# Performance work log

Hardware: AMD Instinct MI355X
Metric: run time of the kernel (lower is better)

The kernel has to match this reference:

```python
import jax, jax.numpy as jnp
import numpy as np

B, D, K, H = 8192, 1024, 8, 2048


def setup_inputs() -> dict:
    key = jax.random.key(0)
    ks = jax.random.split(key, 4)
    x = jax.random.normal(ks[0], (B, D), dtype=jnp.float32)
    centroids = jax.random.normal(ks[1], (K, D), dtype=jnp.float32)
    W1 = jax.random.normal(ks[2], (K, D, H), dtype=jnp.float32) / np.sqrt(D).astype(np.float32)
    b1 = jnp.zeros((K, H), dtype=jnp.float32)
    W2 = jax.random.normal(ks[3], (K, H), dtype=jnp.float32) / np.sqrt(H).astype(np.float32)
    b2 = jnp.zeros((K,), dtype=jnp.float32)
    return {"x": x, "centroids": centroids, "W1": W1, "b1": b1, "W2": W2, "b2": b2}


def reference(x, centroids, W1, b1, W2, b2):
    # --- k-means hard routing: nearest centroid per sample (euclidean max_sim) ---
    # d2[b,k] = ||x_b||^2 - 2 x_b . c_k + ||c_k||^2  (avoid [B,K,D] blowup)
    d2 = (jnp.sum(x * x, axis=-1, keepdims=True)
          - 2.0 * (x @ centroids.T)
          + jnp.sum(centroids * centroids, axis=-1)[None, :])  # [B, K]
    cluster = jnp.argmin(d2, axis=-1)  # [B] int, hard assignment

    # --- per-expert log-likelihood heads (Einet stand-in), computed densely ---
    h = jnp.tanh(jnp.einsum("bd,kdh->kbh", x, W1) + b1[:, None, :])  # [K, B, H]
    lls = jnp.einsum("kbh,kh->kb", h, W2) + b2[:, None]              # [K, B]

    # --- combine: each sample takes the LL from its routed expert, original order ---
    lls_sorted = jnp.take_along_axis(lls.T, cluster[:, None], axis=1)[:, 0]  # [B]
    return lls_sorted
```

## Files before the change

### kernel.cpp

```cpp
#include <hip/hip_runtime.h>
#include <hip/hip_bf16.h>
#include <stdint.h>

#define B_N 8192
#define D_N 1024
#define K_N 8
#define H_N 2048

#define BM 160
#define BN 128
#define BK 64
#define NBLK 512
#define ABYTES 20480
#define BUFSZ 36864
#define RO_OFF 73728
#define PLL_OFF 74368
#define GEMM_LDS 75648

typedef unsigned int u32;
typedef unsigned short u16;
typedef __attribute__((ext_vector_type(8))) short short8;
typedef __attribute__((ext_vector_type(4))) float float4v;

struct __align__(8) us4 { u16 x, y, z, w; };

__device__ __forceinline__ u16 f2bf(float f) {
    union { float f; u32 u; } v; v.f = f;
    u32 u = v.u;
    u32 r = (u + 0x7fffu + ((u >> 16) & 1u)) >> 16;
    return (u16)r;
}

__device__ __forceinline__ float fast_tanh(float x) {
    float t = __expf(2.0f * x);
    return 1.0f - 2.0f * __builtin_amdgcn_rcpf(t + 1.0f);
}

__device__ __forceinline__ void async_copy16(void* lds, const void* g) {
    __builtin_amdgcn_global_load_lds(
        (const __attribute__((address_space(1))) void*)g,
        (__attribute__((address_space(3))) void*)lds, 16, 0, 0);
}

__global__ void route_kernel(const float* __restrict__ x,
                             const float* __restrict__ cent,
                             u16* __restrict__ xbf,
                             int* __restrict__ cluster,
                             u32* __restrict__ counts) {
    int tid = threadIdx.x;
    if (blockIdx.x == 0 && tid < K_N) counts[tid * 32] = 0;
    int wave = tid >> 6, lane = tid & 63;
    int b = blockIdx.x * 4 + wave;
    const float* xr = x + (size_t)b * D_N;

    float4 xv[4];
#pragma unroll
    for (int i = 0; i < 4; ++i)
        xv[i] = *(const float4*)(xr + i * 256 + lane * 4);

#pragma unroll
    for (int i = 0; i < 4; ++i) {
        us4 o;
        o.x = f2bf(xv[i].x); o.y = f2bf(xv[i].y);
        o.z = f2bf(xv[i].z); o.w = f2bf(xv[i].w);
        *(us4*)(xbf + (size_t)b * D_N + i * 256 + lane * 4) = o;
    }

    double acc[K_N];
#pragma unroll
    for (int k = 0; k < K_N; ++k) {
        const float* cr = cent + k * D_N;
        double s = 0.0;
#pragma unroll
        for (int i = 0; i < 4; ++i) {
            float4 cv = *(const float4*)(cr + i * 256 + lane * 4);
            double d0 = (double)xv[i].x - (double)cv.x; s += d0 * d0;
            double d1 = (double)xv[i].y - (double)cv.y; s += d1 * d1;
            double d2 = (double)xv[i].z - (double)cv.z; s += d2 * d2;
            double d3 = (double)xv[i].w - (double)cv.w; s += d3 * d3;
        }
        acc[k] = s;
    }
#pragma unroll
    for (int k = 0; k < K_N; ++k) {
        double v = acc[k];
        for (int off = 32; off; off >>= 1) v += __shfl_down(v, off);
        acc[k] = v;
    }
    if (lane == 0) {
        int best = 0; double bv = acc[0];
#pragma unroll
        for (int k = 1; k < K_N; ++k)
            if (acc[k] < bv) { bv = acc[k]; best = k; }
        cluster[b] = best;
    }
}

__global__ void scatter_kernel(const int* __restrict__ cluster,
                               u32* __restrict__ counts,
                               u32* __restrict__ idxl) {
    __shared__ u32 wcnt[4][K_N];
    __shared__ u32 gb[K_N];
    int tid = threadIdx.x;
    int b = blockIdx.x * 256 + tid;
    int lane = tid & 63, wid = tid >> 6;
    int cl = cluster[b];
    unsigned long long lower = (1ull << lane) - 1ull;
    u32 rank = 0;
#pragma unroll
    for (int k = 0; k < K_N; ++k) {
        unsigned long long mk = __ballot(cl == k);
        if (k == cl) rank = (u32)__popcll(mk & lower);
        if (lane == 0) wcnt[wid][k] = (u32)__popcll(mk);
    }
    __syncthreads();
    if (tid < K_N) {
        u32 tot = wcnt[0][tid] + wcnt[1][tid] + wcnt[2][tid] + wcnt[3][tid];
        gb[tid] = atomicAdd(&counts[tid * 32], tot);
    }
    __syncthreads();
    u32 woff = 0;
    if (wid > 0) woff += wcnt[0][cl];
    if (wid > 1) woff += wcnt[1][cl];
    if (wid > 2) woff += wcnt[2][cl];
    idxl[(size_t)cl * B_N + gb[cl] + woff + rank] = (u32)b;
}

__global__ void w1t_kernel(const float* __restrict__ w1, u16* __restrict__ w1t) {
    __shared__ float ts[64][65];
    int tid = threadIdx.x;
    int h0 = blockIdx.x * 64, d0 = blockIdx.y * 64, k = blockIdx.z;
    const float* src = w1 + ((size_t)k * D_N + d0) * H_N + h0;
#pragma unroll
    for (int i = 0; i < 4; ++i) {
        int q = i * 256 + tid;
        int r = q >> 4, c4 = (q & 15) * 4;
        float4 v = *(const float4*)(src + (size_t)r * H_N + c4);
        ts[c4 + 0][r] = v.x; ts[c4 + 1][r] = v.y;
        ts[c4 + 2][r] = v.z; ts[c4 + 3][r] = v.w;
    }
    __syncthreads();
    u16* dst = w1t + ((size_t)k * H_N + h0) * D_N + d0;
#pragma unroll
    for (int i = 0; i < 4; ++i) {
        int q = i * 256 + tid;
        int hr = q >> 4, d4 = (q & 15) * 4;
        us4 o;
        o.x = f2bf(ts[hr][d4 + 0]); o.y = f2bf(ts[hr][d4 + 1]);
        o.z = f2bf(ts[hr][d4 + 2]); o.w = f2bf(ts[hr][d4 + 3]);
        *(us4*)(dst + (size_t)hr * D_N + d4) = o;
    }
}

__global__ __launch_bounds__(256, 2) void gemm_kernel(
                            const u16* __restrict__ xbf,
                            const u16* __restrict__ w1t,
                            const float* __restrict__ b1,
                            const float* __restrict__ w2,
                            const u32* __restrict__ idxl,
                            const u32* __restrict__ counts,
                            float* __restrict__ llp) {
    extern __shared__ char lds[];
    int tid = threadIdx.x;
    int lane = tid & 63, w = tid >> 6;
    int wm = w >> 1, wn = w & 1;
    int wmbase = wm * 80;
    int l15 = lane & 15, l4 = lane >> 4;

    u32* ro = (u32*)(lds + RO_OFF);
    float* pll = (float*)(lds + PLL_OFF);

    int ntiles = 0;
#pragma unroll
    for (int kk = 0; kk < K_N; ++kk)
        ntiles += ((int)counts[kk * 32] + BM - 1) / BM;
    int total = ntiles * 16;

    int swz = l15 & 7;
    u32 aB0 = (u32)((wmbase + l15) * 128 + (((0 + l4) ^ swz) << 4));
    u32 aB1 = (u32)((wmbase + l15) * 128 + (((4 + l4) ^ swz) << 4));
    u32 bB0 = (u32)(ABYTES + (wn * 64 + l15) * 128 + (((0 + l4) ^ swz) << 4));
    u32 bB1 = (u32)(ABYTES + (wn * 64 + l15) * 128 + (((4 + l4) ^ swz) << 4));

    const char* xb = (const char*)xbf;
    const char* wb = (const char*)w1t;

#define BAR() do { asm volatile("" ::: "memory"); __builtin_amdgcn_s_barrier(); \
                   asm volatile("" ::: "memory"); } while (0)

    for (int item = blockIdx.x; item < total; item += NBLK) {
        int nc = ((item & 7) << 1) | ((item >> 3) & 1);
        int tile = item >> 4;
        int k = 0, mt = 0, nt = 0;
#pragma unroll
        for (int kk = 0; kk < K_N; ++kk) {
            int c = (int)counts[kk * 32];
            int t = (c + BM - 1) / BM;
            if (tile >= nt && tile < nt + t) { k = kk; mt = tile - nt; }
            nt += t;
        }
        int cnt = (int)counts[k * 32];
        int rows = cnt - mt * BM; if (rows > BM) rows = BM;
        int h0 = nc * BN;

        if (tid < BM) {
            int m = mt * BM + tid;
            int mm = m < cnt ? m : cnt - 1;
            ro[tid] = idxl[(size_t)k * B_N + mm] * (u32)(D_N * 2);
        }
        __syncthreads();

        u32 srcA[5], srcB[4];
#pragma unroll
        for (int i = 0; i < 5; ++i) {
            int c = i * 256 + tid; int r = c >> 3, j = c & 7;
            srcA[i] = ro[r] + ((u32)(j ^ (r & 7)) << 4);
        }
#pragma unroll
        for (int i = 0; i < 4; ++i) {
            int c = i * 256 + tid; int r = c >> 3, j = c & 7;
            srcB[i] = ((u32)(k * H_N + h0 + r) << 11) + ((u32)(j ^ (r & 7)) << 4);
        }

        float4v acc[5][4];
#pragma unroll
        for (int mf = 0; mf < 5; ++mf)
#pragma unroll
            for (int nf = 0; nf < 4; ++nf)
                acc[mf][nf] = (float4v){0.f, 0.f, 0.f, 0.f};

#pragma unroll
        for (int i = 0; i < 5; ++i)
            async_copy16(lds + i * 4096 + tid * 16, xb + srcA[i]);
#pragma unroll
        for (int i = 0; i < 4; ++i)
            async_copy16(lds + ABYTES + i * 4096 + tid * 16, wb + srcB[i]);

        for (int t = 0; t < 16; ++t) {
            const char* Acur = lds + (t & 1) * BUFSZ;
            char* Bnx = lds + ((t + 1) & 1) * BUFSZ;
            if (t < 15) {
                u32 d = (u32)((t + 1) << 7);
#pragma unroll
                for (int i = 0; i < 5; ++i)
                    async_copy16(Bnx + i * 4096 + tid * 16, xb + srcA[i] + d);
#pragma unroll
                for (int i = 0; i < 4; ++i)
                    async_copy16(Bnx + ABYTES + i * 4096 + tid * 16, wb + srcB[i] + d);
                asm volatile("s_waitcnt vmcnt(9)" ::: "memory");
            } else {
                asm volatile("s_waitcnt vmcnt(0)" ::: "memory");
            }
            BAR();
#pragma unroll
            for (int kk = 0; kk < 2; ++kk) {
                short8 bC[4], a[5];
                u32 aB = kk ? aB1 : aB0, bB = kk ? bB1 : bB0;
#pragma unroll
                for (int nf = 0; nf < 4; ++nf)
                    bC[nf] = *(const short8*)(Acur + bB + nf * 2048);
#pragma unroll
                for (int mf = 0; mf < 5; ++mf)
                    a[mf] = *(const short8*)(Acur + aB + mf * 2048);
                __builtin_amdgcn_s_setprio(1);
#pragma unroll
                for (int mf = 0; mf < 5; ++mf) {
                    if (wmbase + mf * 16 < rows) {
#pragma unroll
                        for (int nf = 0; nf < 4; ++nf)
                            acc[mf][nf] = __builtin_amdgcn_mfma_f32_16x16x32_bf16(
                                a[mf], bC[nf], acc[mf][nf], 0, 0, 0);
                    }
                }
                __builtin_amdgcn_s_setprio(0);
            }
            BAR();
        }

        float w2v[4], b1v[4];
#pragma unroll
        for (int nf = 0; nf < 4; ++nf) {
            int h = h0 + wn * 64 + nf * 16 + l15;
            w2v[nf] = w2[k * H_N + h];
            b1v[nf] = b1[k * H_N + h];
        }
#pragma unroll
        for (int mf = 0; mf < 5; ++mf) {
            float rs[4] = {0.f, 0.f, 0.f, 0.f};
#pragma unroll
            for (int nf = 0; nf < 4; ++nf) {
#pragma unroll
                for (int r = 0; r < 4; ++r)
                    rs[r] += fast_tanh(acc[mf][nf][r] + b1v[nf]) * w2v[nf];
            }
#pragma unroll
            for (int r = 0; r < 4; ++r) {
                float v = rs[r];
                v += __shfl_xor(v, 8);
                v += __shfl_xor(v, 4);
                v += __shfl_xor(v, 2);
                v += __shfl_xor(v, 1);
                if (l15 == 0) pll[wn * 160 + wmbase + mf * 16 + l4 * 4 + r] = v;
            }
        }
        __syncthreads();
        if (tid < BM) {
            int m = mt * BM + tid;
            if (m < cnt) {
                u32 b = idxl[(size_t)k * B_N + m];
                llp[(size_t)nc * B_N + b] = pll[tid] + pll[160 + tid];
            }
        }
        __syncthreads();
    }
#undef BAR
}

__global__ void combine_kernel(const float* __restrict__ llp,
                               const int* __restrict__ cluster,
                               const float* __restrict__ b2,
                               float* __restrict__ out) {
    int b = blockIdx.x * 256 + threadIdx.x;
    float s = b2[cluster[b]];
#pragma unroll
    for (int nc = 0; nc < 16; ++nc) s += llp[(size_t)nc * B_N + b];
    out[b] = s;
}

extern "C" void kernel_launch(void* const* d_in, const int* in_sizes, int n_in,
                              void* d_out, int out_size, void* d_ws, size_t ws_size,
                              hipStream_t stream) {
    const float* x    = (const float*)d_in[0];
    const float* cent = (const float*)d_in[1];
    const float* W1   = (const float*)d_in[2];
    const float* b1   = (const float*)d_in[3];
    const float* W2   = (const float*)d_in[4];
    const float* b2   = (const float*)d_in[5];
    float* out = (float*)d_out;

    char* ws = (char*)d_ws;
    u16* xbf     = (u16*)(ws + 0);
    u16* w1t     = (u16*)(ws + 16777216);
    u32* counts  = (u32*)(ws + 50331648);
    int* cluster = (int*)(ws + 50332672);
    u32* idxl    = (u32*)(ws + 50365440);
    float* llp   = (float*)(ws + 50627584);

    (void)hipFuncSetAttribute((const void*)gemm_kernel,
                              hipFuncAttributeMaxDynamicSharedMemorySize, GEMM_LDS);

    hipLaunchKernelGGL(route_kernel, dim3(B_N / 4), dim3(256), 0, stream,
                       x, cent, xbf, cluster, counts);
    hipLaunchKernelGGL(scatter_kernel, dim3(32), dim3(256), 0, stream,
                       cluster, counts, idxl);
    hipLaunchKernelGGL(w1t_kernel, dim3(H_N / 64, D_N / 64, K_N), dim3(256), 0, stream,
                       W1, w1t);
    hipLaunchKernelGGL(gemm_kernel, dim3(NBLK), dim3(256), GEMM_LDS, stream,
                       xbf, w1t, b1, W2, idxl, counts, llp);
    hipLaunchKernelGGL(combine_kernel, dim3(B_N / 256), dim3(256), 0, stream,
                       llp, cluster, b2, out);
}
```

Before: 95.87 us.

## Enlarge GEMM tiles to 288x256 with 8 waves and 4-stage half-K pipeline

The GEMM now uses 512-thread blocks with a 288x256 output tile and 32-wide K steps held in a four-deep LDS ring, prefetching two steps ahead. Loads for the next A and B half-stages are interleaved between two MFMA phases inside each step. Larger tiles mean fewer items and less duplicated global traffic for x and W1, and combine now sums 8 partials instead of 16. The trade-offs are higher register pressure from 9x4 accumulators, more LDS per block with fewer blocks resident, and more barriers per K step.

```diff
diff --git a/kernel.cpp b/kernel.cpp
--- a/kernel.cpp
+++ b/kernel.cpp
@@ -7,15 +7,14 @@
 #define K_N 8
 #define H_N 2048
 
-#define BM 160
-#define BN 128
-#define BK 64
-#define NBLK 512
-#define ABYTES 20480
-#define BUFSZ 36864
-#define RO_OFF 73728
-#define PLL_OFF 74368
-#define GEMM_LDS 75648
+#define BM 288
+#define BN 256
+#define NBLK 256
+#define ABYTES_HS 18432
+#define HSB 34816
+#define RO_OFF 139264
+#define PLL_OFF 140416
+#define GEMM_LDS 145024
 
 typedef unsigned int u32;
 typedef unsigned short u16;
@@ -152,7 +151,7 @@
     }
 }
 
-__global__ __launch_bounds__(256, 2) void gemm_kernel(
+__global__ __launch_bounds__(512, 2) void gemm_kernel(
                             const u16* __restrict__ xbf,
                             const u16* __restrict__ w1t,
                             const float* __restrict__ b1,
@@ -163,8 +162,8 @@
     extern __shared__ char lds[];
     int tid = threadIdx.x;
     int lane = tid & 63, w = tid >> 6;
-    int wm = w >> 1, wn = w & 1;
-    int wmbase = wm * 80;
+    int wm = w >> 2, wn = w & 3;
+    int wmbase = wm * 144;
     int l15 = lane & 15, l4 = lane >> 4;
 
     u32* ro = (u32*)(lds + RO_OFF);
@@ -174,23 +173,22 @@
 #pragma unroll
     for (int kk = 0; kk < K_N; ++kk)
         ntiles += ((int)counts[kk * 32] + BM - 1) / BM;
-    int total = ntiles * 16;
-
-    int swz = l15 & 7;
-    u32 aB0 = (u32)((wmbase + l15) * 128 + (((0 + l4) ^ swz) << 4));
-    u32 aB1 = (u32)((wmbase + l15) * 128 + (((4 + l4) ^ swz) << 4));
-    u32 bB0 = (u32)(ABYTES + (wn * 64 + l15) * 128 + (((0 + l4) ^ swz) << 4));
-    u32 bB1 = (u32)(ABYTES + (wn * 64 + l15) * 128 + (((4 + l4) ^ swz) << 4));
+    int total = ntiles * 8;
+
+    int swz = l15 & 3;
+    u32 aBase = (u32)((wmbase + l15) * 64 + ((l4 ^ swz) << 4));
+    u32 bBase = (u32)(ABYTES_HS + (wn * 64 + l15) * 64 + ((l4 ^ swz) << 4));
 
     const char* xb = (const char*)xbf;
     const char* wb = (const char*)w1t;
 
 #define BAR() do { asm volatile("" ::: "memory"); __builtin_amdgcn_s_barrier(); \
                    asm volatile("" ::: "memory"); } while (0)
+#define LGKM0_PIN() do { asm volatile("s_waitcnt lgkmcnt(0)" ::: "memory"); \
+                         __builtin_amdgcn_sched_barrier(0); } while (0)
 
     for (int item = blockIdx.x; item < total; item += NBLK) {
-        int nc = ((item & 7) << 1) | ((item >> 3) & 1);
-        int tile = item >> 4;
+        int tile = item >> 3, nc = item & 7;
         int k = 0, mt = 0, nt = 0;
 #pragma unroll
         for (int kk = 0; kk < K_N; ++kk) {
@@ -210,71 +208,96 @@
         }
         __syncthreads();
 
-        u32 srcA[5], srcB[4];
-#pragma unroll
-        for (int i = 0; i < 5; ++i) {
-            int c = i * 256 + tid; int r = c >> 3, j = c & 7;
-            srcA[i] = ro[r] + ((u32)(j ^ (r & 7)) << 4);
-        }
-#pragma unroll
-        for (int i = 0; i < 4; ++i) {
-            int c = i * 256 + tid; int r = c >> 3, j = c & 7;
-            srcB[i] = ((u32)(k * H_N + h0 + r) << 11) + ((u32)(j ^ (r & 7)) << 4);
-        }
-
-        float4v acc[5][4];
-#pragma unroll
-        for (int mf = 0; mf < 5; ++mf)
+        u32 srcA[3], srcB[2];
+#pragma unroll
+        for (int i = 0; i < 2; ++i) {
+            int c = i * 512 + tid; int r = c >> 2, j = c & 3;
+            srcA[i] = ro[r] + ((u32)(j ^ (r & 3)) << 4);
+        }
+        if (w < 2) {
+            int c = 1024 + tid; int r = c >> 2, j = c & 3;
+            srcA[2] = ro[r] + ((u32)(j ^ (r & 3)) << 4);
+        } else srcA[2] = 0;
+#pragma unroll
+        for (int i = 0; i < 2; ++i) {
+            int c = i * 512 + tid; int r = c >> 2, j = c & 3;
+            srcB[i] = ((u32)(k * H_N + h0 + r) << 11) + ((u32)(j ^ (r & 3)) << 4);
+        }
+
+        float4v acc[9][4];
+#pragma unroll
+        for (int mf = 0; mf < 9; ++mf)
 #pragma unroll
             for (int nf = 0; nf < 4; ++nf)
                 acc[mf][nf] = (float4v){0.f, 0.f, 0.f, 0.f};
 
-#pragma unroll
-        for (int i = 0; i < 5; ++i)
-            async_copy16(lds + i * 4096 + tid * 16, xb + srcA[i]);
-#pragma unroll
-        for (int i = 0; i < 4; ++i)
-            async_copy16(lds + ABYTES + i * 4096 + tid * 16, wb + srcB[i]);
-
-        for (int t = 0; t < 16; ++t) {
-            const char* Acur = lds + (t & 1) * BUFSZ;
-            char* Bnx = lds + ((t + 1) & 1) * BUFSZ;
-            if (t < 15) {
-                u32 d = (u32)((t + 1) << 7);
-#pragma unroll
-                for (int i = 0; i < 5; ++i)
-                    async_copy16(Bnx + i * 4096 + tid * 16, xb + srcA[i] + d);
-#pragma unroll
-                for (int i = 0; i < 4; ++i)
-                    async_copy16(Bnx + ABYTES + i * 4096 + tid * 16, wb + srcB[i] + d);
-                asm volatile("s_waitcnt vmcnt(9)" ::: "memory");
+        auto stageA = [&](int tt) {
+            char* Bp = lds + (tt & 3) * HSB;
+            u32 d = (u32)(tt << 6);
+            async_copy16(Bp + tid * 16,         xb + srcA[0] + d);
+            async_copy16(Bp + 8192 + tid * 16,  xb + srcA[1] + d);
+            if (w < 2)
+                async_copy16(Bp + 16384 + tid * 16, xb + srcA[2] + d);
+        };
+        auto stageB = [&](int tt) {
+            char* Bp = lds + (tt & 3) * HSB + ABYTES_HS;
+            u32 d = (u32)(tt << 6);
+            async_copy16(Bp + tid * 16,         wb + srcB[0] + d);
+            async_copy16(Bp + 8192 + tid * 16,  wb + srcB[1] + d);
+        };
+
+        stageA(0); stageB(0);
+        stageA(1); stageB(1);
+
+        for (int t = 0; t < 32; ++t) {
+            const char* buf = lds + (t & 3) * HSB;
+            bool pre = (t < 30);
+            if (t < 31) {
+                if (w < 2) asm volatile("s_waitcnt vmcnt(5)" ::: "memory");
+                else       asm volatile("s_waitcnt vmcnt(4)" ::: "memory");
             } else {
                 asm volatile("s_waitcnt vmcnt(0)" ::: "memory");
             }
             BAR();
-#pragma unroll
-            for (int kk = 0; kk < 2; ++kk) {
-                short8 bC[4], a[5];
-                u32 aB = kk ? aB1 : aB0, bB = kk ? bB1 : bB0;
-#pragma unroll
-                for (int nf = 0; nf < 4; ++nf)
-                    bC[nf] = *(const short8*)(Acur + bB + nf * 2048);
-#pragma unroll
-                for (int mf = 0; mf < 5; ++mf)
-                    a[mf] = *(const short8*)(Acur + aB + mf * 2048);
-                __builtin_amdgcn_s_setprio(1);
-#pragma unroll
-                for (int mf = 0; mf < 5; ++mf) {
-                    if (wmbase + mf * 16 < rows) {
-#pragma unroll
-                        for (int nf = 0; nf < 4; ++nf)
-                            acc[mf][nf] = __builtin_amdgcn_mfma_f32_16x16x32_bf16(
-                                a[mf], bC[nf], acc[mf][nf], 0, 0, 0);
-                    }
+
+            short8 a[9], bC[4];
+#pragma unroll
+            for (int nf = 0; nf < 4; ++nf)
+                bC[nf] = *(const short8*)(buf + bBase + nf * 1024);
+#pragma unroll
+            for (int mf = 0; mf < 5; ++mf)
+                a[mf] = *(const short8*)(buf + aBase + mf * 1024);
+            if (pre) stageA(t + 2);
+            LGKM0_PIN();
+            __builtin_amdgcn_s_setprio(1);
+#pragma unroll
+            for (int mf = 0; mf < 5; ++mf) {
+                if (wmbase + mf * 16 < rows) {
+#pragma unroll
+                    for (int nf = 0; nf < 4; ++nf)
+                        acc[mf][nf] = __builtin_amdgcn_mfma_f32_16x16x32_bf16(
+                            a[mf], bC[nf], acc[mf][nf], 0, 0, 0);
                 }
-                __builtin_amdgcn_s_setprio(0);
-            }
+            }
+            __builtin_amdgcn_s_setprio(0);
             BAR();
+
+#pragma unroll
+            for (int mf = 5; mf < 9; ++mf)
+                a[mf] = *(const short8*)(buf + aBase + mf * 1024);
+            if (pre) stageB(t + 2);
+            LGKM0_PIN();
+            __builtin_amdgcn_s_setprio(1);
+#pragma unroll
+            for (int mf = 5; mf < 9; ++mf) {
+                if (wmbase + mf * 16 < rows) {
+#pragma unroll
+                    for (int nf = 0; nf < 4; ++nf)
+                        acc[mf][nf] = __builtin_amdgcn_mfma_f32_16x16x32_bf16(
+                            a[mf], bC[nf], acc[mf][nf], 0, 0, 0);
+                }
+            }
+            __builtin_amdgcn_s_setprio(0);
         }
 
         float w2v[4], b1v[4];
@@ -285,7 +308,7 @@
             b1v[nf] = b1[k * H_N + h];
         }
 #pragma unroll
-        for (int mf = 0; mf < 5; ++mf) {
+        for (int mf = 0; mf < 9; ++mf) {
             float rs[4] = {0.f, 0.f, 0.f, 0.f};
 #pragma unroll
             for (int nf = 0; nf < 4; ++nf) {
@@ -300,7 +323,7 @@
                 v += __shfl_xor(v, 4);
                 v += __shfl_xor(v, 2);
                 v += __shfl_xor(v, 1);
-                if (l15 == 0) pll[wn * 160 + wmbase + mf * 16 + l4 * 4 + r] = v;
+                if (l15 == 0) pll[wn * 288 + wmbase + mf * 16 + l4 * 4 + r] = v;
             }
         }
         __syncthreads();
@@ -308,12 +331,13 @@
             int m = mt * BM + tid;
             if (m < cnt) {
                 u32 b = idxl[(size_t)k * B_N + m];
-                llp[(size_t)nc * B_N + b] = pll[tid] + pll[160 + tid];
+                llp[(size_t)nc * B_N + b] = pll[tid] + pll[288 + tid] + pll[576 + tid] + pll[864 + tid];
             }
         }
         __syncthreads();
     }
 #undef BAR
+#undef LGKM0_PIN
 }
 
 __global__ void combine_kernel(const float* __restrict__ llp,
@@ -323,7 +347,7 @@
     int b = blockIdx.x * 256 + threadIdx.x;
     float s = b2[cluster[b]];
 #pragma unroll
-    for (int nc = 0; nc < 16; ++nc) s += llp[(size_t)nc * B_N + b];
+    for (int nc = 0; nc < 8; ++nc) s += llp[(size_t)nc * B_N + b];
     out[b] = s;
 }
 
@@ -355,7 +379,7 @@
                        cluster, counts, idxl);
     hipLaunchKernelGGL(w1t_kernel, dim3(H_N / 64, D_N / 64, K_N), dim3(256), 0, stream,
                        W1, w1t);
-    hipLaunchKernelGGL(gemm_kernel, dim3(NBLK), dim3(256), GEMM_LDS, stream,
+    hipLaunchKernelGGL(gemm_kernel, dim3(NBLK), dim3(512), GEMM_LDS, stream,
                        xbf, w1t, b1, W2, idxl, counts, llp);
     hipLaunchKernelGGL(combine_kernel, dim3(B_N / 256), dim3(256), 0, stream,
                        llp, cluster, b2, out);
```

New measurement: 111.2 us. 1.16x slower.
